# Kernel optimization log

Hardware: AMD Instinct MI355X
Metric: run time of the kernel (lower is better)

The kernel has to match this reference:

```python
import jax, jax.numpy as jnp
import numpy as np
from jax import lax

B, C, H, W = 16, 128, 96, 96  # dim = C


def conv2d(x, w, b, pad, groups=1):
    y = lax.conv_general_dilated(
        x, w, window_strides=(1, 1), padding=[(pad, pad), (pad, pad)],
        dimension_numbers=("NCHW", "OIHW", "NCHW"), feature_group_count=groups)
    return y + b[None, :, None, None]


def setup_inputs() -> dict:
    key = jax.random.key(0)
    ks = jax.random.split(key, 16)
    std = 0.02
    inp = {
        "x": jax.random.normal(ks[0], (B, C, H, W), jnp.float32),
        "sin": jax.random.normal(ks[1], (H * W, C), jnp.float32),
        "cos": jax.random.normal(ks[2], (H * W, C), jnp.float32),
        # qkvo: 1x1 conv, dim -> 4*dim
        "w_qkvo": jax.random.normal(ks[3], (4 * C, C, 1, 1), jnp.float32) * std,
        "b_qkvo": jnp.zeros((4 * C,), jnp.float32),
        # lepe: 5x5 depthwise conv
        "w_lepe": jax.random.normal(ks[4], (C, 1, 5, 5), jnp.float32) * std,
        "b_lepe": jnp.zeros((C,), jnp.float32),
        # proj: 1x1 conv
        "w_proj": jax.random.normal(ks[5], (C, C, 1, 1), jnp.float32) * std,
        "b_proj": jnp.zeros((C,), jnp.float32),
        # 3x3 depthwise convs on q/k/v
        "w_q": jax.random.normal(ks[6], (C, 1, 3, 3), jnp.float32) * std,
        "b_q": jnp.zeros((C,), jnp.float32),
        "w_k": jax.random.normal(ks[7], (C, 1, 3, 3), jnp.float32) * std,
        "b_k": jnp.zeros((C,), jnp.float32),
        "w_v": jax.random.normal(ks[8], (C, 1, 3, 3), jnp.float32) * std,
        "b_v": jnp.zeros((C,), jnp.float32),
    }
    return inp


def reference(x, sin, cos, w_qkvo, b_qkvo, w_lepe, b_lepe, w_proj, b_proj,
              w_q, b_q, w_k, b_k, w_v, b_v):
    # sin/cos are accepted but unused, matching the original forward.
    b, c, h, w = x.shape
    hw = h * w
    scale = c ** (-0.5)

    qkvo = conv2d(x, w_qkvo, b_qkvo, 0)          # (B, 4C, H, W)
    qkv = qkvo[:, :3 * c]
    o = qkvo[:, 3 * c:]
    lepe = conv2d(qkv[:, 2 * c:], w_lepe, b_lepe, 2, groups=c)  # (B, C, H, W)

    q = qkv[:, :c]
    k = qkv[:, c:2 * c]
    v = qkv[:, 2 * c:]
    q = q + conv2d(q, w_q, b_q, 1, groups=c)
    k = k + conv2d(k, w_k, b_k, 1, groups=c)
    v = v + conv2d(v, w_v, b_v, 1, groups=c)

    # (B, C, H, W) -> (B, HW, C)
    to_tok = lambda t: t.reshape(b, c, hw).transpose(0, 2, 1)
    q = jax.nn.elu(to_tok(q)) + 1.0
    k = jax.nn.elu(to_tok(k)) + 1.0
    v = to_tok(v)

    k_mean = k.mean(axis=1, keepdims=True)                    # (B, 1, C)
    z = jnp.einsum("bnc,bmc->bnm", q, k_mean) * scale         # (B, HW, 1)

    s = (scale / hw) ** 0.5
    kv = jnp.einsum("bnc,bnd->bcd", k * s, v * s)             # (B, C, C)

    res = (jnp.einsum("bnc,bcd->bnd", q, kv) * (1.0 + 1.0 / (z + 1e-6))
           - z * v.mean(axis=2, keepdims=True))               # (B, HW, C)

    res = res.transpose(0, 2, 1).reshape(b, c, h, w)
    res = res + lepe
    return conv2d(res * o, w_proj, b_proj, 0)
```

## Files before the change

kernel.cpp:

```cpp
#include <hip/hip_runtime.h>
#include <math.h>

#define HW 9216
#define BSTRIDE_QKVO ((size_t)4718592)
#define BSTRIDE_C    ((size_t)1179648)
#define KVS 24

typedef __attribute__((ext_vector_type(4))) short short4v;
typedef __attribute__((ext_vector_type(8))) short short8v;
typedef __attribute__((ext_vector_type(4))) float f32x4;
typedef __attribute__((ext_vector_type(4))) unsigned short u16x4;

__device__ __forceinline__ unsigned short f2b(float f) {
  union { float f; unsigned u; } v; v.f = f;
  unsigned r = (v.u + 0x7fffu + ((v.u >> 16) & 1u)) >> 16;
  return (unsigned short)r;
}
__device__ __forceinline__ float b2f(unsigned short h) {
  union { unsigned u; float f; } v; v.u = ((unsigned)h) << 16;
  return v.f;
}
__device__ __forceinline__ int xswz(int x, int nx) {
  return (x & 7) * (nx >> 3) + (x >> 3);
}

__global__ void cvt_kernel(const float* __restrict__ in, unsigned short* __restrict__ out, int n) {
  int i = blockIdx.x * 256 + threadIdx.x;
  if (i < n) out[i] = f2b(in[i]);
}

template<int BSRC_F32, int OUT_F32, int NOCB>
__global__ __launch_bounds__(256) void gemm_k128s(
    const unsigned short* __restrict__ A, const void* __restrict__ Bv,
    const float* __restrict__ bias, void* __restrict__ Ov,
    size_t bstrB, size_t bstrO)
{
  __shared__ unsigned short Bt[128 * 132];
  const int t = threadIdx.x, lane = t & 63, wave = t >> 6;
  const int wr = wave >> 1, wc = wave & 1;
  const int l4 = lane & 15, lg = lane >> 4;
  const int pb = xswz(blockIdx.x, 72) << 7, b = blockIdx.y;

  if (BSRC_F32) {
    const float* B = (const float*)Bv + (size_t)b * bstrB;
    #pragma unroll
    for (int i = 0; i < 8; ++i) {
      int id = t + (i << 8);
      int kp = id >> 5, pg = id & 31;
      const float* r0 = B + (size_t)(2 * kp) * HW + pb + (pg << 2);
      f32x4 a = *(const f32x4*)r0;
      f32x4 c = *(const f32x4*)(r0 + HW);
      #pragma unroll
      for (int j = 0; j < 4; ++j)
        *(unsigned*)&Bt[((pg << 2) + j) * 132 + 2 * kp] =
            (unsigned)f2b(a[j]) | ((unsigned)f2b(c[j]) << 16);
    }
  } else {
    const unsigned short* B = (const unsigned short*)Bv + (size_t)b * bstrB;
    #pragma unroll
    for (int i = 0; i < 8; ++i) {
      int id = t + (i << 8);
      int kp = id >> 5, pg = id & 31;
      const unsigned short* r0 = B + (size_t)(2 * kp) * HW + pb + (pg << 2);
      u16x4 a = *(const u16x4*)r0;
      u16x4 c = *(const u16x4*)(r0 + HW);
      #pragma unroll
      for (int j = 0; j < 4; ++j)
        *(unsigned*)&Bt[((pg << 2) + j) * 132 + 2 * kp] =
            (unsigned)a[j] | ((unsigned)c[j] << 16);
    }
  }

  __syncthreads();

  short8v af[4][4];
  #pragma unroll
  for (int mp = 0; mp < 4; ++mp)
    #pragma unroll
    for (int ks = 0; ks < 4; ++ks) {
      int base = (wr * 64 + mp * 16 + l4) * 132 + ks * 32 + lg * 8;
      short4v lo = *(const short4v*)&Bt[base];
      short4v hi = *(const short4v*)&Bt[base + 4];
      short8v v;
      v[0] = lo[0]; v[1] = lo[1]; v[2] = lo[2]; v[3] = lo[3];
      v[4] = hi[0]; v[5] = hi[1]; v[6] = hi[2]; v[7] = hi[3];
      af[mp][ks] = v;
    }

  for (int co = 0; co < NOCB; ++co) {
    f32x4 acc[4][4];
    #pragma unroll
    for (int mp = 0; mp < 4; ++mp)
      #pragma unroll
      for (int nd = 0; nd < 4; ++nd) acc[mp][nd] = (f32x4){0.f, 0.f, 0.f, 0.f};

    #pragma unroll
    for (int ks = 0; ks < 4; ++ks) {
      short8v bfk[4];
      #pragma unroll
      for (int nd = 0; nd < 4; ++nd)
        bfk[nd] = *(const short8v*)(A + (size_t)(co * 128 + wc * 64 + nd * 16 + l4) * 128 + ks * 32 + lg * 8);
      #pragma unroll
      for (int nd = 0; nd < 4; ++nd)
        #pragma unroll
        for (int mp = 0; mp < 4; ++mp)
          acc[mp][nd] = __builtin_amdgcn_mfma_f32_16x16x32_bf16(af[mp][ks], bfk[nd], acc[mp][nd], 0, 0, 0);
    }

    float bb[4];
    #pragma unroll
    for (int nd = 0; nd < 4; ++nd) bb[nd] = bias[co * 128 + wc * 64 + nd * 16 + l4];

    if (OUT_F32) {
      float* O = (float*)Ov + (size_t)b * bstrO;
      #pragma unroll
      for (int mp = 0; mp < 4; ++mp) {
        int px = pb + wr * 64 + mp * 16 + lg * 4;
        #pragma unroll
        for (int nd = 0; nd < 4; ++nd) {
          int oc = co * 128 + wc * 64 + nd * 16 + l4;
          f32x4 v;
          #pragma unroll
          for (int i = 0; i < 4; ++i) v[i] = acc[mp][nd][i] + bb[nd];
          *(f32x4*)&O[(size_t)oc * HW + px] = v;
        }
      }
    } else {
      unsigned short* O = (unsigned short*)Ov + (size_t)b * bstrO;
      #pragma unroll
      for (int mp = 0; mp < 4; ++mp) {
        int px = pb + wr * 64 + mp * 16 + lg * 4;
        #pragma unroll
        for (int nd = 0; nd < 4; ++nd) {
          int oc = co * 128 + wc * 64 + nd * 16 + l4;
          u16x4 v;
          #pragma unroll
          for (int i = 0; i < 4; ++i) v[i] = f2b(acc[mp][nd][i] + bb[nd]);
          *(u16x4*)&O[(size_t)oc * HW + px] = v;
        }
      }
    }
  }
}

__device__ __forceinline__ void stage_plane(const unsigned short* __restrict__ g,
                                            float* __restrict__ sp, int t) {
  #pragma unroll
  for (int i = 0; i < 9; ++i) {
    int f = (t + (i << 8)) << 2;
    u16x4 u = *(const u16x4*)&g[f];
    f32x4 fv;
    fv[0] = b2f(u[0]); fv[1] = b2f(u[1]); fv[2] = b2f(u[2]); fv[3] = b2f(u[3]);
    *(f32x4*)&sp[f] = fv;
  }
}

__device__ __forceinline__ f32x4 conv3_strip(const float* __restrict__ sp, int base,
                                             const float* __restrict__ w9,
                                             bool j0, bool j23, f32x4* cen) {
  f32x4 acc = (f32x4){0.f, 0.f, 0.f, 0.f};
  #pragma unroll
  for (int ky = 0; ky < 3; ++ky) {
    const float* rowp = sp + base + (ky - 1) * 96;
    f32x4 w0 = *(const f32x4*)(rowp - 4);
    f32x4 w1 = *(const f32x4*)(rowp);
    f32x4 w2 = *(const f32x4*)(rowp + 4);
    float xm1 = j0 ? 0.f : w0[3];
    float xp4 = j23 ? 0.f : w2[0];
    float k0 = w9[ky * 3], k1 = w9[ky * 3 + 1], k2 = w9[ky * 3 + 2];
    acc[0] += k0 * xm1   + k1 * w1[0] + k2 * w1[1];
    acc[1] += k0 * w1[0] + k1 * w1[1] + k2 * w1[2];
    acc[2] += k0 * w1[1] + k1 * w1[2] + k2 * w1[3];
    acc[3] += k0 * w1[2] + k1 * w1[3] + k2 * xp4;
    if (ky == 1) *cen = w1;
  }
  return acc;
}

__global__ __launch_bounds__(256) void dwconv_kernel(
    unsigned short* __restrict__ qkvo,
    const float* __restrict__ w_q, const float* __restrict__ b_q,
    const float* __restrict__ w_k, const float* __restrict__ b_k,
    const float* __restrict__ w_v, const float* __restrict__ b_v,
    const float* __restrict__ w_lepe, const float* __restrict__ b_lepe,
    unsigned short* __restrict__ lp, float* __restrict__ ksum)
{
  __shared__ float sb[9612];
  __shared__ float red[256];
  const int c = blockIdx.x, b = blockIdx.y, t = threadIdx.x;
  unsigned short* qg = qkvo + ((size_t)b * 512 + c) * HW;
  unsigned short* kg = qg + (size_t)128 * HW;
  unsigned short* vg = qg + (size_t)256 * HW;
  unsigned short* lg = lp + ((size_t)b * 128 + c) * HW;
  float* sp = sb + 196;

  for (int i = t; i < 384; i += 256) {
    int idx = (i < 192) ? (i - 192) : (9024 + i);
    sp[idx] = 0.f;
  }

  {
    stage_plane(qg, sp, t);
    float w9[9];
    #pragma unroll
    for (int i = 0; i < 9; ++i) w9[i] = w_q[c * 9 + i];
    float bb = b_q[c];
    __syncthreads();
    for (int i = 0; i < 9; ++i) {
      int s = t + (i << 8);
      int r = s / 24, j = s - r * 24;
      int base = r * 96 + (j << 2);
      f32x4 cen;
      f32x4 a = conv3_strip(sp, base, w9, j == 0, j == 23, &cen);
      u16x4 o;
      #pragma unroll
      for (int k = 0; k < 4; ++k) {
        float v = cen[k] + bb + a[k];
        o[k] = f2b(v > 0.f ? v + 1.f : __expf(v));
      }
      *(u16x4*)&qg[base] = o;
    }
    __syncthreads();
  }
  float kacc = 0.f;
  {
    stage_plane(kg, sp, t);
    float w9[9];
    #pragma unroll
    for (int i = 0; i < 9; ++i) w9[i] = w_k[c * 9 + i];
    float bb = b_k[c];
    __syncthreads();
    for (int i = 0; i < 9; ++i) {
      int s = t + (i << 8);
      int r = s / 24, j = s - r * 24;
      int base = r * 96 + (j << 2);
      f32x4 cen;
      f32x4 a = conv3_strip(sp, base, w9, j == 0, j == 23, &cen);
      u16x4 o;
      #pragma unroll
      for (int k = 0; k < 4; ++k) {
        float v = cen[k] + bb + a[k];
        float e = v > 0.f ? v + 1.f : __expf(v);
        o[k] = f2b(e);
        kacc += e;
      }
      *(u16x4*)&kg[base] = o;
    }
    __syncthreads();
  }
  {
    stage_plane(vg, sp, t);
    float w9[9], w25[25];
    #pragma unroll
    for (int i = 0; i < 9; ++i) w9[i] = w_v[c * 9 + i];
    #pragma unroll
    for (int i = 0; i < 25; ++i) w25[i] = w_lepe[c * 25 + i];
    float bv = b_v[c], bl = b_lepe[c];
    __syncthreads();
    for (int i = 0; i < 9; ++i) {
      int s = t + (i << 8);
      int r = s / 24, j = s - r * 24;
      int base = r * 96 + (j << 2);
      bool j0 = (j == 0), j23 = (j == 23);
      f32x4 a3 = (f32x4){0.f, 0.f, 0.f, 0.f};
      f32x4 a5 = (f32x4){0.f, 0.f, 0.f, 0.f};
      f32x4 cen = (f32x4){0.f, 0.f, 0.f, 0.f};
      #pragma unroll
      for (int ky = 0; ky < 5; ++ky) {
        const float* rowp = sp + base + (ky - 2) * 96;
        f32x4 w0 = *(const f32x4*)(rowp - 4);
        f32x4 w1 = *(const f32x4*)(rowp);
        f32x4 w2 = *(const f32x4*)(rowp + 4);
        float xm2 = j0 ? 0.f : w0[2];
        float xm1 = j0 ? 0.f : w0[3];
        float xp4 = j23 ? 0.f : w2[0];
        float xp5 = j23 ? 0.f : w2[1];
        const float* wr5 = w25 + ky * 5;
        a5[0] += wr5[0]*xm2   + wr5[1]*xm1   + wr5[2]*w1[0] + wr5[3]*w1[1] + wr5[4]*w1[2];
        a5[1] += wr5[0]*xm1   + wr5[1]*w1[0] + wr5[2]*w1[1] + wr5[3]*w1[2] + wr5[4]*w1[3];
        a5[2] += wr5[0]*w1[0] + wr5[1]*w1[1] + wr5[2]*w1[2] + wr5[3]*w1[3] + wr5[4]*xp4;
        a5[3] += wr5[0]*w1[1] + wr5[1]*w1[2] + wr5[2]*w1[3] + wr5[3]*xp4   + wr5[4]*xp5;
        if (ky >= 1 && ky <= 3) {
          float k0 = w9[(ky-1)*3], k1 = w9[(ky-1)*3+1], k2 = w9[(ky-1)*3+2];
          a3[0] += k0 * xm1   + k1 * w1[0] + k2 * w1[1];
          a3[1] += k0 * w1[0] + k1 * w1[1] + k2 * w1[2];
          a3[2] += k0 * w1[1] + k1 * w1[2] + k2 * w1[3];
          a3[3] += k0 * w1[2] + k1 * w1[3] + k2 * xp4;
          if (ky == 2) cen = w1;
        }
      }
      u16x4 o, lo16;
      #pragma unroll
      for (int k = 0; k < 4; ++k) {
        o[k] = f2b(cen[k] + bv + a3[k]);
        lo16[k] = f2b(bl + a5[k]);
      }
      *(u16x4*)&vg[base] = o;
      *(u16x4*)&lg[base] = lo16;
    }
  }
  red[t] = kacc; __syncthreads();
  for (int s2 = 128; s2 > 0; s2 >>= 1) { if (t < s2) red[t] += red[t + s2]; __syncthreads(); }
  if (t == 0) ksum[b * 128 + c] = red[0];
}

__global__ __launch_bounds__(256) void kv_mfma(
    const unsigned short* __restrict__ qkvo, float* __restrict__ part,
    float* __restrict__ vmean)
{
  __shared__ float vml[2][384];
  const int t = threadIdx.x, lane = t & 63, wave = t >> 6;
  const int wr = wave >> 1, wc = wave & 1;
  const int l4 = lane & 15, lg = lane >> 4;
  const int s = xswz(blockIdx.x, KVS), b = blockIdx.y;
  const unsigned short* kbase = qkvo + (size_t)b * BSTRIDE_QKVO + (size_t)128 * HW;
  const unsigned short* vbase = kbase + (size_t)128 * HW;
  const int p0 = s * 384;

  f32x4 acc[4][4];
  #pragma unroll
  for (int m = 0; m < 4; ++m)
    #pragma unroll
    for (int n = 0; n < 4; ++n) acc[m][n] = (f32x4){0.f, 0.f, 0.f, 0.f};

  for (int kk = 0; kk < 12; ++kk) {
    int p = p0 + kk * 32 + lg * 8;
    short8v ka[4], va[4];
    #pragma unroll
    for (int m = 0; m < 4; ++m) ka[m] = *(const short8v*)(kbase + (size_t)(wr * 64 + m * 16 + l4) * HW + p);
    #pragma unroll
    for (int n = 0; n < 4; ++n) va[n] = *(const short8v*)(vbase + (size_t)(wc * 64 + n * 16 + l4) * HW + p);

    if (wr == 0) {
      float pv[8];
      #pragma unroll
      for (int e = 0; e < 8; ++e) {
        pv[e] = b2f((unsigned short)va[0][e]) + b2f((unsigned short)va[1][e])
              + b2f((unsigned short)va[2][e]) + b2f((unsigned short)va[3][e]);
        #pragma unroll
        for (int m2 = 1; m2 < 16; m2 <<= 1)
          pv[e] += __shfl_xor(pv[e], m2, 64);
      }
      if (l4 == 0) {
        #pragma unroll
        for (int e = 0; e < 8; ++e) vml[wc][kk * 32 + lg * 8 + e] = pv[e];
      }
    }

    #pragma unroll
    for (int n = 0; n < 4; ++n)
      #pragma unroll
      for (int m = 0; m < 4; ++m)
        acc[m][n] = __builtin_amdgcn_mfma_f32_16x16x32_bf16(ka[m], va[n], acc[m][n], 0, 0, 0);
  }

  float* pp = part + ((size_t)b * KVS + s) * 16384;
  #pragma unroll
  for (int m = 0; m < 4; ++m)
    #pragma unroll
    for (int n = 0; n < 4; ++n) {
      int d = wc * 64 + n * 16 + l4;
      #pragma unroll
      for (int i = 0; i < 4; ++i) {
        int cch = wr * 64 + m * 16 + lg * 4 + i;
        pp[(cch << 7) + d] = acc[m][n][i];
      }
    }

  __syncthreads();
  for (int i = t; i < 384; i += 256)
    vmean[(size_t)b * HW + p0 + i] = (vml[0][i] + vml[1][i]) * (1.f / 128.f);
}

__global__ void kvreduce(const float* __restrict__ part, unsigned short* __restrict__ kvT) {
  const int b = blockIdx.y;
  const int e0 = blockIdx.x * 2048 + threadIdx.x;
  const float* pb_ = part + (size_t)b * KVS * 16384;
  for (int i = 0; i < 8; ++i) {
    int e = e0 + i * 256;
    int cch = e >> 7, d = e & 127;
    float sum = 0.f;
    #pragma unroll 8
    for (int s = 0; s < KVS; ++s) sum += pb_[(size_t)s * 16384 + e];
    kvT[(size_t)b * 16384 + d * 128 + cch] = f2b(sum);
  }
}

__global__ __launch_bounds__(256) void attn_proj(
    const unsigned short* __restrict__ qkvo, const unsigned short* __restrict__ kvT,
    const float* __restrict__ ksum, const float* __restrict__ vmean,
    const unsigned short* __restrict__ lp, const unsigned short* __restrict__ wph,
    const float* __restrict__ b_proj, float* __restrict__ outp)
{
  __shared__ unsigned short Bt[128 * 132];
  __shared__ float zb[128];
  __shared__ float km[128];
  const int t = threadIdx.x, lane = t & 63, wave = t >> 6;
  const int wr = wave >> 1, wc = wave & 1;
  const int l4 = lane & 15, lg = lane >> 4;
  const int pb = xswz(blockIdx.x, 72) << 7, b = blockIdx.y;
  const float kSCf = (float)(0.08838834764831843 / 9216.0);

  const unsigned short* qs = qkvo + (size_t)b * BSTRIDE_QKVO;
  const unsigned short* os = qs + (size_t)384 * HW;
  const unsigned short* lpb = lp + (size_t)b * BSTRIDE_C;
  float* ob = outp + (size_t)b * BSTRIDE_C;

  if (t < 128) km[t] = ksum[(b << 7) + t];

  #pragma unroll
  for (int i = 0; i < 8; ++i) {
    int id = t + (i << 8);
    int kp = id >> 5, pg = id & 31;
    const unsigned short* r0 = qs + (size_t)(2 * kp) * HW + pb + (pg << 2);
    u16x4 a = *(const u16x4*)r0;
    u16x4 c = *(const u16x4*)(r0 + HW);
    #pragma unroll
    for (int j = 0; j < 4; ++j)
      *(unsigned*)&Bt[((pg << 2) + j) * 132 + 2 * kp] =
          (unsigned)a[j] | ((unsigned)c[j] << 16);
  }

  const unsigned short* Ab = kvT + (size_t)b * 16384;
  short8v bkv[4][4];
  #pragma unroll
  for (int nd = 0; nd < 4; ++nd)
    #pragma unroll
    for (int ks = 0; ks < 4; ++ks)
      bkv[nd][ks] = *(const short8v*)(Ab + (size_t)(wc * 64 + nd * 16 + l4) * 128 + ks * 32 + lg * 8);

  f32x4 acc[4][4];
  #pragma unroll
  for (int mp = 0; mp < 4; ++mp)
    #pragma unroll
    for (int nd = 0; nd < 4; ++nd) acc[mp][nd] = (f32x4){0.f, 0.f, 0.f, 0.f};

  __syncthreads();

  if (t < 128) {
    float za = 0.f;
    #pragma unroll 8
    for (int cch = 0; cch < 128; ++cch) za += b2f(Bt[t * 132 + cch]) * km[cch];
    zb[t] = za;
  }

  #pragma unroll
  for (int ks = 0; ks < 4; ++ks) {
    short8v aq[4];
    #pragma unroll
    for (int mp = 0; mp < 4; ++mp) {
      int base = (wr * 64 + mp * 16 + l4) * 132 + ks * 32 + lg * 8;
      short4v lo = *(const short4v*)&Bt[base];
      short4v hi = *(const short4v*)&Bt[base + 4];
      short8v v;
      v[0] = lo[0]; v[1] = lo[1]; v[2] = lo[2]; v[3] = lo[3];
      v[4] = hi[0]; v[5] = hi[1]; v[6] = hi[2]; v[7] = hi[3];
      aq[mp] = v;
    }
    #pragma unroll
    for (int nd = 0; nd < 4; ++nd)
      #pragma unroll
      for (int mp = 0; mp < 4; ++mp)
        acc[mp][nd] = __builtin_amdgcn_mfma_f32_16x16x32_bf16(aq[mp], bkv[nd][ks], acc[mp][nd], 0, 0, 0);
  }

  __syncthreads();

  #pragma unroll
  for (int mp = 0; mp < 4; ++mp) {
    int pxl = wr * 64 + mp * 16 + lg * 4;
    int px = pb + pxl;
    f32x4 zv = *(const f32x4*)&zb[pxl];
    f32x4 vm = *(const f32x4*)&vmean[(size_t)b * HW + px];
    f32x4 zfv, zvmv;
    #pragma unroll
    for (int i = 0; i < 4; ++i) {
      float z = zv[i] * kSCf;
      zfv[i]  = kSCf * (1.f + 1.f / (z + 1e-6f));
      zvmv[i] = z * vm[i];
    }
    #pragma unroll
    for (int nd = 0; nd < 4; ++nd) {
      int d = wc * 64 + nd * 16 + l4;
      u16x4 lev = *(const u16x4*)&lpb[(size_t)d * HW + px];
      u16x4 ovv = *(const u16x4*)&os[(size_t)d * HW + px];
      #pragma unroll
      for (int i = 0; i < 4; ++i) {
        float r = (acc[mp][nd][i] * zfv[i] - zvmv[i] + b2f(lev[i])) * b2f(ovv[i]);
        Bt[(pxl + i) * 132 + d] = f2b(r);
      }
    }
  }

  __syncthreads();

  f32x4 acc2[4][4];
  #pragma unroll
  for (int mp = 0; mp < 4; ++mp)
    #pragma unroll
    for (int nd = 0; nd < 4; ++nd) acc2[mp][nd] = (f32x4){0.f, 0.f, 0.f, 0.f};

  #pragma unroll
  for (int ks = 0; ks < 4; ++ks) {
    short8v aq[4];
    #pragma unroll
    for (int mp = 0; mp < 4; ++mp) {
      int base = (wr * 64 + mp * 16 + l4) * 132 + ks * 32 + lg * 8;
      short4v lo = *(const short4v*)&Bt[base];
      short4v hi = *(const short4v*)&Bt[base + 4];
      short8v v;
      v[0] = lo[0]; v[1] = lo[1]; v[2] = lo[2]; v[3] = lo[3];
      v[4] = hi[0]; v[5] = hi[1]; v[6] = hi[2]; v[7] = hi[3];
      aq[mp] = v;
    }
    short8v pw[4];
    #pragma unroll
    for (int nd = 0; nd < 4; ++nd)
      pw[nd] = *(const short8v*)(wph + (size_t)(wc * 64 + nd * 16 + l4) * 128 + ks * 32 + lg * 8);
    #pragma unroll
    for (int nd = 0; nd < 4; ++nd)
      #pragma unroll
      for (int mp = 0; mp < 4; ++mp)
        acc2[mp][nd] = __builtin_amdgcn_mfma_f32_16x16x32_bf16(aq[mp], pw[nd], acc2[mp][nd], 0, 0, 0);
  }

  float bb[4];
  #pragma unroll
  for (int nd = 0; nd < 4; ++nd) bb[nd] = b_proj[wc * 64 + nd * 16 + l4];

  #pragma unroll
  for (int mp = 0; mp < 4; ++mp) {
    int px = pb + wr * 64 + mp * 16 + lg * 4;
    #pragma unroll
    for (int nd = 0; nd < 4; ++nd) {
      int oc = wc * 64 + nd * 16 + l4;
      f32x4 v;
      #pragma unroll
      for (int i = 0; i < 4; ++i) v[i] = acc2[mp][nd][i] + bb[nd];
      *(f32x4*)&ob[(size_t)oc * HW + px] = v;
    }
  }
}

extern "C" void kernel_launch(void* const* d_in, const int* in_sizes, int n_in,
                              void* d_out, int out_size, void* d_ws, size_t ws_size,
                              hipStream_t stream) {
  const float* x      = (const float*)d_in[0];
  const float* w_qkvo = (const float*)d_in[3];
  const float* b_qkvo = (const float*)d_in[4];
  const float* w_lepe = (const float*)d_in[5];
  const float* b_lepe = (const float*)d_in[6];
  const float* w_proj = (const float*)d_in[7];
  const float* b_proj = (const float*)d_in[8];
  const float* w_q = (const float*)d_in[9];
  const float* b_q = (const float*)d_in[10];
  const float* w_k = (const float*)d_in[11];
  const float* b_k = (const float*)d_in[12];
  const float* w_v = (const float*)d_in[13];
  const float* b_v = (const float*)d_in[14];
  float* out = (float*)d_out;

  unsigned short* wqh = (unsigned short*)d_ws;
  unsigned short* wph = wqh + 65536;
  const size_t perb_bytes = 9437184 + 1572864 + 32768 + 512 + 36864 + 2359296;
  int G = 0;
  for (int g = 16; g >= 1; g >>= 1)
    if ((size_t)163840 + (size_t)g * perb_bytes <= ws_size) { G = g; break; }
  if (G == 0) return;

  size_t off = 163840;
  unsigned short* qkvo_h = (unsigned short*)((char*)d_ws + off); off += (size_t)G * 9437184;
  float* kvpart = (float*)((char*)d_ws + off);                   off += (size_t)G * 1572864;
  unsigned short* kvT = (unsigned short*)((char*)d_ws + off);    off += (size_t)G * 32768;
  float* ksum = (float*)((char*)d_ws + off);                     off += (size_t)G * 512;
  float* vmeanp = (float*)((char*)d_ws + off);                   off += (size_t)G * 36864;
  unsigned short* lepe_h = (unsigned short*)((char*)d_ws + off);

  cvt_kernel<<<dim3(256), 256, 0, stream>>>(w_qkvo, wqh, 65536);
  cvt_kernel<<<dim3(64),  256, 0, stream>>>(w_proj, wph, 16384);

  for (int b0 = 0; b0 < 16; b0 += G) {
    const float* xc  = x   + (size_t)b0 * BSTRIDE_C;
    float*       oc_ = out + (size_t)b0 * BSTRIDE_C;

    gemm_k128s<1, 0, 4><<<dim3(72, G), 256, 0, stream>>>(
        wqh, xc, b_qkvo, qkvo_h, BSTRIDE_C, BSTRIDE_QKVO);
    dwconv_kernel<<<dim3(128, G), 256, 0, stream>>>(qkvo_h, w_q, b_q, w_k, b_k, w_v, b_v,
                                                    w_lepe, b_lepe, lepe_h, ksum);
    kv_mfma<<<dim3(KVS, G), 256, 0, stream>>>(qkvo_h, kvpart, vmeanp);
    kvreduce<<<dim3(8, G), 256, 0, stream>>>(kvpart, kvT);
    attn_proj<<<dim3(72, G), 256, 0, stream>>>(qkvo_h, kvT, ksum, vmeanp, lepe_h,
                                               wph, b_proj, oc_);
  }
}
```

Before: 271.5 us.

## Recompute o-projection inside attn_proj instead of storing it from the qkvo GEMM

The first GEMM now produces only q, k and v, so the o channels are no longer written to or read back from a bf16 workspace. attn_proj instead loads the fp32 input x tile, converts it to bf16 in shared memory, and computes o with an extra MFMA pass using the last quarter of the qkvo weights plus bias. This removes a write and read of B*C*HW bf16 values in exchange for reading the fp32 input again and doing extra LDS staging and a sync. The kv-weight register loads move into the k-loop to cut register pressure, and the final output store becomes nontemporal.

```diff
diff --git a/kernel.cpp b/kernel.cpp
--- a/kernel.cpp
+++ b/kernel.cpp
@@ -2,7 +2,7 @@
 #include <math.h>
 
 #define HW 9216
-#define BSTRIDE_QKVO ((size_t)4718592)
+#define BSTRIDE_QKV  ((size_t)3538944)
 #define BSTRIDE_C    ((size_t)1179648)
 #define KVS 24
 
@@ -188,7 +188,7 @@
   __shared__ float sb[9612];
   __shared__ float red[256];
   const int c = blockIdx.x, b = blockIdx.y, t = threadIdx.x;
-  unsigned short* qg = qkvo + ((size_t)b * 512 + c) * HW;
+  unsigned short* qg = qkvo + ((size_t)b * 384 + c) * HW;
   unsigned short* kg = qg + (size_t)128 * HW;
   unsigned short* vg = qg + (size_t)256 * HW;
   unsigned short* lg = lp + ((size_t)b * 128 + c) * HW;
@@ -313,7 +313,7 @@
   const int wr = wave >> 1, wc = wave & 1;
   const int l4 = lane & 15, lg = lane >> 4;
   const int s = xswz(blockIdx.x, KVS), b = blockIdx.y;
-  const unsigned short* kbase = qkvo + (size_t)b * BSTRIDE_QKVO + (size_t)128 * HW;
+  const unsigned short* kbase = qkvo + (size_t)b * BSTRIDE_QKV + (size_t)128 * HW;
   const unsigned short* vbase = kbase + (size_t)128 * HW;
   const int p0 = s * 384;
 
@@ -387,10 +387,13 @@
 }
 
 __global__ __launch_bounds__(256) void attn_proj(
-    const unsigned short* __restrict__ qkvo, const unsigned short* __restrict__ kvT,
+    const unsigned short* __restrict__ qkvo, const float* __restrict__ xin,
+    const unsigned short* __restrict__ kvT,
     const float* __restrict__ ksum, const float* __restrict__ vmean,
-    const unsigned short* __restrict__ lp, const unsigned short* __restrict__ wph,
-    const float* __restrict__ b_proj, float* __restrict__ outp)
+    const unsigned short* __restrict__ lp,
+    const unsigned short* __restrict__ woh, const float* __restrict__ b_o,
+    const unsigned short* __restrict__ wph, const float* __restrict__ b_proj,
+    float* __restrict__ outp)
 {
   __shared__ unsigned short Bt[128 * 132];
   __shared__ float zb[128];
@@ -401,12 +404,60 @@
   const int pb = xswz(blockIdx.x, 72) << 7, b = blockIdx.y;
   const float kSCf = (float)(0.08838834764831843 / 9216.0);
 
-  const unsigned short* qs = qkvo + (size_t)b * BSTRIDE_QKVO;
-  const unsigned short* os = qs + (size_t)384 * HW;
+  const unsigned short* qs = qkvo + (size_t)b * BSTRIDE_QKV;
   const unsigned short* lpb = lp + (size_t)b * BSTRIDE_C;
   float* ob = outp + (size_t)b * BSTRIDE_C;
 
   if (t < 128) km[t] = ksum[(b << 7) + t];
+
+  {
+    const float* B = xin + (size_t)b * BSTRIDE_C;
+    #pragma unroll
+    for (int i = 0; i < 8; ++i) {
+      int id = t + (i << 8);
+      int kp = id >> 5, pg = id & 31;
+      const float* r0 = B + (size_t)(2 * kp) * HW + pb + (pg << 2);
+      f32x4 a = *(const f32x4*)r0;
+      f32x4 c = *(const f32x4*)(r0 + HW);
+      #pragma unroll
+      for (int j = 0; j < 4; ++j)
+        *(unsigned*)&Bt[((pg << 2) + j) * 132 + 2 * kp] =
+            (unsigned)f2b(a[j]) | ((unsigned)f2b(c[j]) << 16);
+    }
+  }
+  __syncthreads();
+
+  f32x4 acco[4][4];
+  #pragma unroll
+  for (int mp = 0; mp < 4; ++mp)
+    #pragma unroll
+    for (int nd = 0; nd < 4; ++nd) acco[mp][nd] = (f32x4){0.f, 0.f, 0.f, 0.f};
+
+  #pragma unroll
+  for (int ks = 0; ks < 4; ++ks) {
+    short8v ax[4];
+    #pragma unroll
+    for (int mp = 0; mp < 4; ++mp) {
+      int base = (wr * 64 + mp * 16 + l4) * 132 + ks * 32 + lg * 8;
+      short4v lo = *(const short4v*)&Bt[base];
+      short4v hi = *(const short4v*)&Bt[base + 4];
+      short8v v;
+      v[0] = lo[0]; v[1] = lo[1]; v[2] = lo[2]; v[3] = lo[3];
+      v[4] = hi[0]; v[5] = hi[1]; v[6] = hi[2]; v[7] = hi[3];
+      ax[mp] = v;
+    }
+    short8v pw[4];
+    #pragma unroll
+    for (int nd = 0; nd < 4; ++nd)
+      pw[nd] = *(const short8v*)(woh + (size_t)(wc * 64 + nd * 16 + l4) * 128 + ks * 32 + lg * 8);
+    #pragma unroll
+    for (int nd = 0; nd < 4; ++nd)
+      #pragma unroll
+      for (int mp = 0; mp < 4; ++mp)
+        acco[mp][nd] = __builtin_amdgcn_mfma_f32_16x16x32_bf16(ax[mp], pw[nd], acco[mp][nd], 0, 0, 0);
+  }
+
+  __syncthreads();
 
   #pragma unroll
   for (int i = 0; i < 8; ++i) {
@@ -421,14 +472,6 @@
           (unsigned)a[j] | ((unsigned)c[j] << 16);
   }
 
-  const unsigned short* Ab = kvT + (size_t)b * 16384;
-  short8v bkv[4][4];
-  #pragma unroll
-  for (int nd = 0; nd < 4; ++nd)
-    #pragma unroll
-    for (int ks = 0; ks < 4; ++ks)
-      bkv[nd][ks] = *(const short8v*)(Ab + (size_t)(wc * 64 + nd * 16 + l4) * 128 + ks * 32 + lg * 8);
-
   f32x4 acc[4][4];
   #pragma unroll
   for (int mp = 0; mp < 4; ++mp)
@@ -444,6 +487,7 @@
     zb[t] = za;
   }
 
+  const unsigned short* Ab = kvT + (size_t)b * 16384;
   #pragma unroll
   for (int ks = 0; ks < 4; ++ks) {
     short8v aq[4];
@@ -457,14 +501,22 @@
       v[4] = hi[0]; v[5] = hi[1]; v[6] = hi[2]; v[7] = hi[3];
       aq[mp] = v;
     }
+    short8v bkv[4];
     #pragma unroll
     for (int nd = 0; nd < 4; ++nd)
+      bkv[nd] = *(const short8v*)(Ab + (size_t)(wc * 64 + nd * 16 + l4) * 128 + ks * 32 + lg * 8);
+    #pragma unroll
+    for (int nd = 0; nd < 4; ++nd)
       #pragma unroll
       for (int mp = 0; mp < 4; ++mp)
-        acc[mp][nd] = __builtin_amdgcn_mfma_f32_16x16x32_bf16(aq[mp], bkv[nd][ks], acc[mp][nd], 0, 0, 0);
+        acc[mp][nd] = __builtin_amdgcn_mfma_f32_16x16x32_bf16(aq[mp], bkv[nd], acc[mp][nd], 0, 0, 0);
   }
 
   __syncthreads();
+
+  float bo[4];
+  #pragma unroll
+  for (int nd = 0; nd < 4; ++nd) bo[nd] = b_o[wc * 64 + nd * 16 + l4];
 
   #pragma unroll
   for (int mp = 0; mp < 4; ++mp) {
@@ -483,10 +535,10 @@
     for (int nd = 0; nd < 4; ++nd) {
       int d = wc * 64 + nd * 16 + l4;
       u16x4 lev = *(const u16x4*)&lpb[(size_t)d * HW + px];
-      u16x4 ovv = *(const u16x4*)&os[(size_t)d * HW + px];
       #pragma unroll
       for (int i = 0; i < 4; ++i) {
-        float r = (acc[mp][nd][i] * zfv[i] - zvmv[i] + b2f(lev[i])) * b2f(ovv[i]);
+        float ov = acco[mp][nd][i] + bo[nd];
+        float r = (acc[mp][nd][i] * zfv[i] - zvmv[i] + b2f(lev[i])) * ov;
         Bt[(pxl + i) * 132 + d] = f2b(r);
       }
     }
@@ -537,7 +589,7 @@
       f32x4 v;
       #pragma unroll
       for (int i = 0; i < 4; ++i) v[i] = acc2[mp][nd][i] + bb[nd];
-      *(f32x4*)&ob[(size_t)oc * HW + px] = v;
+      __builtin_nontemporal_store(v, (f32x4*)&ob[(size_t)oc * HW + px]);
     }
   }
 }
@@ -562,14 +614,14 @@
 
   unsigned short* wqh = (unsigned short*)d_ws;
   unsigned short* wph = wqh + 65536;
-  const size_t perb_bytes = 9437184 + 1572864 + 32768 + 512 + 36864 + 2359296;
+  const size_t perb_bytes = 7077888 + 1572864 + 32768 + 512 + 36864 + 2359296;
   int G = 0;
   for (int g = 16; g >= 1; g >>= 1)
     if ((size_t)163840 + (size_t)g * perb_bytes <= ws_size) { G = g; break; }
   if (G == 0) return;
 
   size_t off = 163840;
-  unsigned short* qkvo_h = (unsigned short*)((char*)d_ws + off); off += (size_t)G * 9437184;
+  unsigned short* qkv_h = (unsigned short*)((char*)d_ws + off);  off += (size_t)G * 7077888;
   float* kvpart = (float*)((char*)d_ws + off);                   off += (size_t)G * 1572864;
   unsigned short* kvT = (unsigned short*)((char*)d_ws + off);    off += (size_t)G * 32768;
   float* ksum = (float*)((char*)d_ws + off);                     off += (size_t)G * 512;
@@ -583,13 +635,14 @@
     const float* xc  = x   + (size_t)b0 * BSTRIDE_C;
     float*       oc_ = out + (size_t)b0 * BSTRIDE_C;
 
-    gemm_k128s<1, 0, 4><<<dim3(72, G), 256, 0, stream>>>(
-        wqh, xc, b_qkvo, qkvo_h, BSTRIDE_C, BSTRIDE_QKVO);
-    dwconv_kernel<<<dim3(128, G), 256, 0, stream>>>(qkvo_h, w_q, b_q, w_k, b_k, w_v, b_v,
+    gemm_k128s<1, 0, 3><<<dim3(72, G), 256, 0, stream>>>(
+        wqh, xc, b_qkvo, qkv_h, BSTRIDE_C, BSTRIDE_QKV);
+    dwconv_kernel<<<dim3(128, G), 256, 0, stream>>>(qkv_h, w_q, b_q, w_k, b_k, w_v, b_v,
                                                     w_lepe, b_lepe, lepe_h, ksum);
-    kv_mfma<<<dim3(KVS, G), 256, 0, stream>>>(qkvo_h, kvpart, vmeanp);
+    kv_mfma<<<dim3(KVS, G), 256, 0, stream>>>(qkv_h, kvpart, vmeanp);
     kvreduce<<<dim3(8, G), 256, 0, stream>>>(kvpart, kvT);
-    attn_proj<<<dim3(72, G), 256, 0, stream>>>(qkvo_h, kvT, ksum, vmeanp, lepe_h,
+    attn_proj<<<dim3(72, G), 256, 0, stream>>>(qkv_h, xc, kvT, ksum, vmeanp, lepe_h,
+                                               wqh + (size_t)384 * 128, b_qkvo + 384,
                                                wph, b_proj, oc_);
   }
 }
```

Result: faster. 265.4 us (-2.2%).
